# Optimization experiments

Hardware: AMD Instinct MI355X
Metric: run time of the kernel (lower is better)

The kernel has to match this reference:

```python
import jax, jax.numpy as jnp
import numpy as np

NUM_HEADS = 32
NUM_KV_HEADS = 8
HEAD_DIM = 128
ROPE_THETA = 10000.0
MAX_SEQ_LEN = 2048


def build_rope_cache(seq_len, head_dim, theta=10000.0):
    freq_indices = jnp.arange(0, head_dim, 2, dtype=jnp.float32)
    inv_freq = 1.0 / theta ** (freq_indices / head_dim)
    positions = jnp.arange(seq_len, dtype=jnp.float32)
    angles = jnp.outer(positions, inv_freq)  # (S, D/2)
    cos = jnp.cos(angles)
    sin = jnp.sin(angles)
    return jnp.concatenate([cos, cos], axis=-1), jnp.concatenate([sin, sin], axis=-1)


def apply_rotary_embedding(x, cos, sin):
    # x: (B, S, H, D); cos/sin: (S, D)
    d = x.shape[-1]
    x1, x2 = x[..., : d // 2], x[..., d // 2 :]
    x_rot = jnp.concatenate([-x2, x1], axis=-1)
    return x * cos[None, :, None, :] + x_rot * sin[None, :, None, :]


def setup_inputs() -> dict:
    key = jax.random.key(0)
    k_x, k_q, k_k, k_v, k_o = jax.random.split(key, 5)
    B, S, HID = 2, 2048, NUM_HEADS * HEAD_DIM
    KV = NUM_KV_HEADS * HEAD_DIM
    x = jax.random.normal(k_x, (B, S, HID), dtype=jnp.float32)
    # causal mask, shape (B, 1, S, S)
    causal = jnp.tril(jnp.ones((S, S), dtype=bool))
    mask = jnp.broadcast_to(causal[None, None], (B, 1, S, S))
    sc_in = 1.0 / np.sqrt(HID)
    Wq = jax.random.normal(k_q, (HID, HID), dtype=jnp.float32) * sc_in
    Wk = jax.random.normal(k_k, (HID, KV), dtype=jnp.float32) * sc_in
    Wv = jax.random.normal(k_v, (HID, KV), dtype=jnp.float32) * sc_in
    Wo = jax.random.normal(k_o, (HID, HID), dtype=jnp.float32) * sc_in
    return {"x": x, "mask": mask, "Wq": Wq, "Wk": Wk, "Wv": Wv, "Wo": Wo}


def reference(x, mask, Wq, Wk, Wv, Wo):
    B, S, _ = x.shape
    q = (x @ Wq).reshape(B, S, NUM_HEADS, HEAD_DIM)
    k = (x @ Wk).reshape(B, S, NUM_KV_HEADS, HEAD_DIM)
    v = (x @ Wv).reshape(B, S, NUM_KV_HEADS, HEAD_DIM)
    cos, sin = build_rope_cache(MAX_SEQ_LEN, HEAD_DIM, ROPE_THETA)
    cos, sin = cos[:S], sin[:S]
    q = apply_rotary_embedding(q, cos, sin)
    k = apply_rotary_embedding(k, cos, sin)
    group = NUM_HEADS // NUM_KV_HEADS
    if group > 1:
        k = jnp.repeat(k, group, axis=2)
        v = jnp.repeat(v, group, axis=2)
    scale = HEAD_DIM ** -0.5
    # (B, H, S, S)
    scores = jnp.einsum("bqhd,bkhd->bhqk", q, k) * scale
    scores = jnp.where(mask, scores, jnp.finfo(jnp.float32).min)
    attn = jax.nn.softmax(scores, axis=-1)
    out = jnp.einsum("bhqk,bkhd->bqhd", attn, v).reshape(B, S, NUM_HEADS * HEAD_DIM)
    return out @ Wo
```

## Files before the change

### kernel.cpp

```cpp
#include <hip/hip_runtime.h>

#define S_LEN   2048
#define HID_DIM 4096
#define NHEADS  32
#define NKVH    8
#define HD      128
#define KV_DIM  1024
#define KV2     2048
#define BS_ROWS 4096

typedef __attribute__((ext_vector_type(4))) float f32x4;
typedef __attribute__((ext_vector_type(8))) short bf16x8;

__device__ __forceinline__ unsigned short f2b(float f) {
  union { float f; unsigned int u; } cv; cv.f = f;
  unsigned int r = (cv.u + 0x7FFFu + ((cv.u >> 16) & 1u)) >> 16;
  return (unsigned short)r;
}
__device__ __forceinline__ float b2f(unsigned short u) {
  union { unsigned int u; float f; } cv; cv.u = ((unsigned int)u) << 16; return cv.f;
}
__device__ __forceinline__ void gload_lds16(const void* g, void* l) {
  __builtin_amdgcn_global_load_lds(
      (const __attribute__((address_space(1))) unsigned int*)g,
      (__attribute__((address_space(3))) unsigned int*)l, 16, 0, 0);
}
__device__ __forceinline__ float exp2fast(float x) {
#if __has_builtin(__builtin_amdgcn_exp2f)
  return __builtin_amdgcn_exp2f(x);
#else
  return exp2f(x);
#endif
}
__device__ __forceinline__ unsigned cvtpk(float a, float b) {
  unsigned r;
  asm("v_cvt_pk_bf16_f32 %0, %1, %2" : "=v"(r) : "v"(a), "v"(b));
  return r;
}
__device__ __forceinline__ void store_out(float* p, float v) { *p = v; }
__device__ __forceinline__ void store_out(unsigned short* p, float v) { *p = f2b(v); }

__global__ __launch_bounds__(256) void prep_k(const float* __restrict__ x,
                                              unsigned short* __restrict__ xb,
                                              const float* __restrict__ Wq,
                                              unsigned short* __restrict__ wtb,
                                              const float* __restrict__ Wk,
                                              unsigned short* __restrict__ wkt,
                                              const float* __restrict__ Wv,
                                              unsigned short* __restrict__ wvt,
                                              float* __restrict__ cosT,
                                              float* __restrict__ sinT) {
  __shared__ float t[32][33];
  int bid = blockIdx.x;
  const int tid = threadIdx.x;
  if (bid < 16384) {
    int i = bid * 256 + tid;
    f32x4 v = reinterpret_cast<const f32x4*>(x)[i];
    ushort4 o;
    o.x = f2b(v[0]); o.y = f2b(v[1]); o.z = f2b(v[2]); o.w = f2b(v[3]);
    reinterpret_cast<ushort4*>(xb)[i] = o;
    return;
  }
  bid -= 16384;
  const float* W; unsigned short* Wt; int Kd, Nd, bx, by;
  if (bid < 16384) { W = Wq; Wt = wtb; Kd = HID_DIM; Nd = HID_DIM; bx = bid & 127; by = bid >> 7; }
  else {
    bid -= 16384;
    if (bid < 4096) { W = Wk; Wt = wkt; Kd = HID_DIM; Nd = KV_DIM; bx = bid & 31; by = bid >> 5; }
    else {
      bid -= 4096;
      if (bid < 4096) { W = Wv; Wt = wvt; Kd = HID_DIM; Nd = KV_DIM; bx = bid & 31; by = bid >> 5; }
      else {
        bid -= 4096;
        int idx = bid * 256 + tid;
        int s = idx >> 6, i = idx & 63;
        float inv = 1.0f / powf(10000.0f, (float)(2 * i) * (1.0f / 128.0f));
        float ang = (float)s * inv;
        cosT[idx] = cosf(ang);
        sinT[idx] = sinf(ang);
        return;
      }
    }
  }
  const int tx = tid & 31, ty = tid >> 5;
  const int n0 = bx * 32, k0 = by * 32;
#pragma unroll
  for (int i = 0; i < 4; ++i)
    t[ty + 8 * i][tx] = W[(size_t)(k0 + ty + 8 * i) * Nd + n0 + tx];
  __syncthreads();
#pragma unroll
  for (int i = 0; i < 4; ++i)
    Wt[(size_t)(n0 + ty + 8 * i) * Kd + k0 + tx] = f2b(t[tx][ty + 8 * i]);
}

__global__ void transpose_cvt(const float* __restrict__ W, unsigned short* __restrict__ Wt,
                              int K, int N) {
  __shared__ float t[32][33];
  int n0 = blockIdx.x * 32, k0 = blockIdx.y * 32;
  int tx = threadIdx.x, ty = threadIdx.y;
#pragma unroll
  for (int i = 0; i < 4; ++i)
    t[ty + 8 * i][tx] = W[(size_t)(k0 + ty + 8 * i) * N + n0 + tx];
  __syncthreads();
#pragma unroll
  for (int i = 0; i < 4; ++i)
    Wt[(size_t)(n0 + ty + 8 * i) * K + k0 + tx] = f2b(t[tx][ty + 8 * i]);
}

__global__ __launch_bounds__(256) void postkv_k(unsigned short* __restrict__ KVb,
                                                unsigned short* __restrict__ Vt,
                                                const float* __restrict__ cosT,
                                                const float* __restrict__ sinT) {
  __shared__ unsigned short tsh[32][33];
  int bid = blockIdx.x;
  const int tid = threadIdx.x;
  if (bid < 2048) {
    int idx = bid * 256 + tid;
    int i4 = idx & 15;
    int t = idx >> 4;
    int h = t & (NKVH - 1);
    int row = t >> 3;
    int s = row & (S_LEN - 1);
    f32x4 c4 = *reinterpret_cast<const f32x4*>(&cosT[(s << 6) + i4 * 4]);
    f32x4 s4 = *reinterpret_cast<const f32x4*>(&sinT[(s << 6) + i4 * 4]);
    size_t base = (size_t)row * KV2 + (size_t)h * HD + i4 * 4;
    ushort4 xa = *reinterpret_cast<const ushort4*>(&KVb[base]);
    ushort4 xb2 = *reinterpret_cast<const ushort4*>(&KVb[base + 64]);
    unsigned short* pa = (unsigned short*)&xa;
    unsigned short* pb = (unsigned short*)&xb2;
    ushort4 oa, ob;
    unsigned short* qa = (unsigned short*)&oa;
    unsigned short* qb = (unsigned short*)&ob;
#pragma unroll
    for (int j = 0; j < 4; ++j) {
      float x1 = b2f(pa[j]), x2 = b2f(pb[j]);
      qa[j] = f2b(x1 * c4[j] - x2 * s4[j]);
      qb[j] = f2b(x2 * c4[j] + x1 * s4[j]);
    }
    *reinterpret_cast<ushort4*>(&KVb[base])      = oa;
    *reinterpret_cast<ushort4*>(&KVb[base + 64]) = ob;
    return;
  }
  bid -= 2048;
  const int tx = tid & 31, ty = tid >> 5;
  int c0 = (bid & 31) * 32;
  int r0 = (bid >> 5) * 32;
#pragma unroll
  for (int i = 0; i < 4; ++i)
    tsh[ty + 8 * i][tx] = KVb[(size_t)(r0 + ty + 8 * i) * KV2 + KV_DIM + c0 + tx];
  __syncthreads();
  int ob2 = (r0 >> 11) * 1024;
  int oc = r0 & 2047;
#pragma unroll
  for (int i = 0; i < 4; ++i)
    Vt[(size_t)(ob2 + c0 + ty + 8 * i) * S_LEN + oc + tx] = tsh[tx][ty + 8 * i];
}

template <typename OutT>
__global__ __launch_bounds__(256) void gemm_bt(const unsigned short* __restrict__ A,
                                               const unsigned short* __restrict__ Bt,
                                               OutT* __restrict__ C, int M, int N, int K) {
  __shared__ unsigned short As[128 * 32];
  __shared__ unsigned short Bs[128 * 32];
  const int tid = threadIdx.x;
  const int lane = tid & 63;
  const int wave = tid >> 6;
  int nwg = gridDim.x, wg = blockIdx.x;
  int swz = (nwg % 8 == 0) ? ((wg & 7) * (nwg >> 3) + (wg >> 3)) : wg;
  const int nbn = N >> 7;
  const int bm = swz / nbn, bn = swz % nbn;
  const int m0 = bm << 7, n0 = bn << 7;
  const int wr = wave >> 1, wc = wave & 1;
  const int lr = lane & 15, kb = lane >> 4;

  f32x4 acc[4][4];
#pragma unroll
  for (int i = 0; i < 4; ++i)
#pragma unroll
    for (int j = 0; j < 4; ++j) acc[i][j] = (f32x4){0.f, 0.f, 0.f, 0.f};

  const unsigned short* Ab = A + (size_t)m0 * K;
  const unsigned short* Bb = Bt + (size_t)n0 * K;

  for (int k0 = 0; k0 < K; k0 += 32) {
    __syncthreads();
#pragma unroll
    for (int i = 0; i < 2; ++i) {
      int idx = i * 256 + tid;
      int row = idx >> 2;
      int off = (idx & 3) << 3;
      gload_lds16(Ab + (size_t)row * K + k0 + off, As + row * 32 + off);
      gload_lds16(Bb + (size_t)row * K + k0 + off, Bs + row * 32 + off);
    }
    __syncthreads();

    bf16x8 af[4], bfr[4];
#pragma unroll
    for (int mi = 0; mi < 4; ++mi)
      af[mi] = *reinterpret_cast<const bf16x8*>(As + (wr * 64 + mi * 16 + lr) * 32 + kb * 8);
#pragma unroll
    for (int ni = 0; ni < 4; ++ni)
      bfr[ni] = *reinterpret_cast<const bf16x8*>(Bs + (wc * 64 + ni * 16 + lr) * 32 + kb * 8);
#pragma unroll
    for (int mi = 0; mi < 4; ++mi)
#pragma unroll
      for (int ni = 0; ni < 4; ++ni)
        acc[mi][ni] = __builtin_amdgcn_mfma_f32_16x16x32_bf16(af[mi], bfr[ni], acc[mi][ni], 0, 0, 0);
  }

#pragma unroll
  for (int mi = 0; mi < 4; ++mi)
#pragma unroll
    for (int ni = 0; ni < 4; ++ni)
#pragma unroll
      for (int r = 0; r < 4; ++r) {
        int row = m0 + wr * 64 + mi * 16 + kb * 4 + r;
        int col = n0 + wc * 64 + ni * 16 + lr;
        store_out(&C[(size_t)row * N + col], acc[mi][ni][r]);
      }
}

#define STAGE_HALF(dstBase, Sp, k0, h)                                           \
  {                                                                              \
    _Pragma("unroll")                                                            \
    for (int i_ = 0; i_ < 2; ++i_) {                                             \
      int c_ = i_ * 512 + tid;                                                   \
      int rl_ = c_ >> 3, ch_ = c_ & 7;                                           \
      int row_ = (h) * 128 + rl_;                                                \
      gload_lds16((Sp) + (size_t)row_ * K + (k0) + ((ch_ ^ (row_ & 7)) << 3),    \
                  (char*)(dstBase) + row_ * 128 + ch_ * 16);                     \
    }                                                                            \
  }
#define LDF(buf, R, sw) \
  (*reinterpret_cast<const bf16x8*>((const char*)(buf) + (R) * 128 + (sw)))
#define PHASE_SYNC()                                        \
  __builtin_amdgcn_s_barrier();                             \
  asm volatile("s_waitcnt lgkmcnt(0)" ::: "memory");        \
  __builtin_amdgcn_sched_barrier(0);

template <typename OutT>
__global__ __launch_bounds__(512, 1) void gemm256(const unsigned short* __restrict__ A,
                                                  const unsigned short* __restrict__ Bt,
                                                  OutT* __restrict__ C, int M, int N, int K) {
  __shared__ unsigned short Asl[2][256 * 64];
  __shared__ unsigned short Bsl[2][256 * 64];
  const int tid = threadIdx.x;
  const int lane = tid & 63;
  const int wave = tid >> 6;
  const int wr = wave >> 2;
  const int wc = wave & 3;
  const int lr = lane & 15, kb = lane >> 4;

  int nwg = gridDim.x, wg = blockIdx.x;
  int swz = (nwg % 8 == 0) ? ((wg & 7) * (nwg >> 3) + (wg >> 3)) : wg;
  const int nbn = N >> 8;
  const int bm = swz / nbn, bn = swz % nbn;
  const int m0 = bm << 8, n0 = bn << 8;

  const unsigned short* Ab = A + (size_t)m0 * K;
  const unsigned short* Bb = Bt + (size_t)n0 * K;

  f32x4 acc[8][4];
#pragma unroll
  for (int i = 0; i < 8; ++i)
#pragma unroll
    for (int j = 0; j < 4; ++j) acc[i][j] = (f32x4){0.f, 0.f, 0.f, 0.f};

  const int sw0 = ((kb) ^ (lr & 7)) << 4;
  const int sw1 = ((4 + kb) ^ (lr & 7)) << 4;

  STAGE_HALF(Asl[0], Ab, 0, 0); STAGE_HALF(Asl[0], Ab, 0, 1);
  STAGE_HALF(Bsl[0], Bb, 0, 0); STAGE_HALF(Bsl[0], Bb, 0, 1);
  __syncthreads();

  const int nt = K >> 6;
  bf16x8 af[4], bfr[4];

#pragma unroll 1
  for (int t = 0; t < nt; ++t) {
    const unsigned short* Acur = Asl[t & 1];
    const unsigned short* Bcur = Bsl[t & 1];
    unsigned short* Anxt = Asl[(t + 1) & 1];
    unsigned short* Bnxt = Bsl[(t + 1) & 1];
    const int k0n = (t + 1) << 6;
    const bool pf = (t + 1 < nt);

#pragma unroll
    for (int ni = 0; ni < 4; ++ni) bfr[ni] = LDF(Bcur, wc * 64 + ni * 16 + lr, sw0);
#pragma unroll
    for (int mi = 0; mi < 4; ++mi) af[mi] = LDF(Acur, wr * 128 + mi * 16 + lr, sw0);
    if (pf) { STAGE_HALF(Anxt, Ab, k0n, 0); STAGE_HALF(Anxt, Ab, k0n, 1); }
    PHASE_SYNC();
    __builtin_amdgcn_s_setprio(1);
#pragma unroll
    for (int mi = 0; mi < 4; ++mi)
#pragma unroll
      for (int ni = 0; ni < 4; ++ni)
        acc[mi][ni] = __builtin_amdgcn_mfma_f32_16x16x32_bf16(af[mi], bfr[ni], acc[mi][ni], 0, 0, 0);
    __builtin_amdgcn_s_setprio(0);
    __builtin_amdgcn_s_barrier();

#pragma unroll
    for (int mi = 0; mi < 4; ++mi) af[mi] = LDF(Acur, wr * 128 + (mi + 4) * 16 + lr, sw0);
    if (pf) { STAGE_HALF(Bnxt, Bb, k0n, 0); STAGE_HALF(Bnxt, Bb, k0n, 1); }
    PHASE_SYNC();
    __builtin_amdgcn_s_setprio(1);
#pragma unroll
    for (int mi = 0; mi < 4; ++mi)
#pragma unroll
      for (int ni = 0; ni < 4; ++ni)
        acc[mi + 4][ni] = __builtin_amdgcn_mfma_f32_16x16x32_bf16(af[mi], bfr[ni], acc[mi + 4][ni], 0, 0, 0);
    __builtin_amdgcn_s_setprio(0);
    __builtin_amdgcn_s_barrier();

#pragma unroll
    for (int ni = 0; ni < 4; ++ni) bfr[ni] = LDF(Bcur, wc * 64 + ni * 16 + lr, sw1);
#pragma unroll
    for (int mi = 0; mi < 4; ++mi) af[mi] = LDF(Acur, wr * 128 + mi * 16 + lr, sw1);
    PHASE_SYNC();
    __builtin_amdgcn_s_setprio(1);
#pragma unroll
    for (int mi = 0; mi < 4; ++mi)
#pragma unroll
      for (int ni = 0; ni < 4; ++ni)
        acc[mi][ni] = __builtin_amdgcn_mfma_f32_16x16x32_bf16(af[mi], bfr[ni], acc[mi][ni], 0, 0, 0);
    __builtin_amdgcn_s_setprio(0);
    __builtin_amdgcn_s_barrier();

#pragma unroll
    for (int mi = 0; mi < 4; ++mi) af[mi] = LDF(Acur, wr * 128 + (mi + 4) * 16 + lr, sw1);
    PHASE_SYNC();
    __builtin_amdgcn_s_setprio(1);
#pragma unroll
    for (int mi = 0; mi < 4; ++mi)
#pragma unroll
      for (int ni = 0; ni < 4; ++ni)
        acc[mi + 4][ni] = __builtin_amdgcn_mfma_f32_16x16x32_bf16(af[mi], bfr[ni], acc[mi + 4][ni], 0, 0, 0);
    __builtin_amdgcn_s_setprio(0);
    __builtin_amdgcn_s_barrier();

    if (pf) asm volatile("s_waitcnt vmcnt(0)" ::: "memory");
    __builtin_amdgcn_s_barrier();
  }

#pragma unroll
  for (int mi = 0; mi < 8; ++mi)
#pragma unroll
    for (int ni = 0; ni < 4; ++ni)
#pragma unroll
      for (int r = 0; r < 4; ++r) {
        int row = m0 + wr * 128 + mi * 16 + kb * 4 + r;
        int col = n0 + wc * 64 + ni * 16 + lr;
        store_out(&C[(size_t)row * N + col], acc[mi][ni][r]);
      }
}

__global__ __launch_bounds__(256, 2) void attn_fwd(const unsigned short* __restrict__ Q,
                                                   const unsigned short* __restrict__ KV,
                                                   const unsigned short* __restrict__ Vt,
                                                   const float* __restrict__ cosT,
                                                   const float* __restrict__ sinT,
                                                   unsigned short* __restrict__ O) {
  __shared__ unsigned short Ks[2][64 * 128];
  __shared__ unsigned short Ps[4][2][16 * 72];
  const int tid = threadIdx.x, lane = tid & 63, wave = tid >> 6;
  const int lr = lane & 15, kb = lane >> 4;
  const int pr = blockIdx.x;
  const int bh = blockIdx.y;
  const int b = bh >> 5, h = bh & 31, kvh = h >> 2;
  const unsigned short* Qp = Q + (size_t)b * S_LEN * HID_DIM + (size_t)h * HD;
  const unsigned short* Kp = KV + (size_t)b * S_LEN * KV2 + (size_t)kvh * HD;
  const unsigned short* Vtp = Vt + (size_t)(b * 8 + kvh) * HD * S_LEN;
  unsigned short* Op = O + (size_t)b * S_LEN * HID_DIM + (size_t)h * HD;

#pragma unroll 1
  for (int pass = 0; pass < 2; ++pass) {
    const int qt = pass ? pr : 15 - pr;
    const int q0 = qt * 128;
    int qrowQ[2];
    qrowQ[0] = q0 + wave * 32 + lr;
    qrowQ[1] = q0 + wave * 32 + 16 + lr;

    bf16x8 qf[2][4];
#pragma unroll
    for (int qs = 0; qs < 2; ++qs) {
      const int qrow = qrowQ[qs];
      bf16x8 raw[4];
#pragma unroll
      for (int dc = 0; dc < 4; ++dc)
        raw[dc] = *reinterpret_cast<const bf16x8*>(Qp + (size_t)qrow * HID_DIM + dc * 32 + kb * 8);
      const float* ct = cosT + (qrow << 6) + kb * 8;
      const float* st = sinT + (qrow << 6) + kb * 8;
      f32x4 cv0 = *(const f32x4*)(ct),      cv1 = *(const f32x4*)(ct + 4);
      f32x4 cv2 = *(const f32x4*)(ct + 32), cv3 = *(const f32x4*)(ct + 36);
      f32x4 sv0 = *(const f32x4*)(st),      sv1 = *(const f32x4*)(st + 4);
      f32x4 sv2 = *(const f32x4*)(st + 32), sv3 = *(const f32x4*)(st + 36);
      const float sc = 0.08838834764831843f * 1.4426950408889634f;
#pragma unroll
      for (int j = 0; j < 8; ++j) {
        const int jj = j & 3;
        float c0 = (j < 4) ? cv0[jj] : cv1[jj];
        float s0 = (j < 4) ? sv0[jj] : sv1[jj];
        float c1 = (j < 4) ? cv2[jj] : cv3[jj];
        float s1 = (j < 4) ? sv2[jj] : sv3[jj];
        float a1 = b2f((unsigned short)raw[0][j]), a2 = b2f((unsigned short)raw[2][j]);
        qf[qs][0][j] = (short)f2b((a1 * c0 - a2 * s0) * sc);
        qf[qs][2][j] = (short)f2b((a2 * c0 + a1 * s0) * sc);
        float b1 = b2f((unsigned short)raw[1][j]), b2x = b2f((unsigned short)raw[3][j]);
        qf[qs][1][j] = (short)f2b((b1 * c1 - b2x * s1) * sc);
        qf[qs][3][j] = (short)f2b((b2x * c1 + b1 * s1) * sc);
      }
    }

    f32x4 of[2][8];
#pragma unroll
    for (int qs = 0; qs < 2; ++qs)
#pragma unroll
      for (int i = 0; i < 8; ++i) of[qs][i] = (f32x4){0.f, 0.f, 0.f, 0.f};
    float mrow[2] = {-3.0e38f, -3.0e38f};
    float lrow[2] = {0.f, 0.f};

    const int nsteps = 2 * qt + 2;

#pragma unroll
    for (int i = 0; i < 4; ++i) {
      int c = i * 256 + tid;
      int key = c >> 4;
      int ch = (c & 15) ^ (key & 7);
      gload_lds16(Kp + (size_t)key * KV2 + ch * 8, &Ks[0][0] + c * 8);
    }
    __syncthreads();

#pragma unroll 1
    for (int t = 0; t < nsteps; ++t) {
      const int kv0 = t << 6;
      const unsigned short* Kcur = &Ks[t & 1][0];
      const bool active = (kv0 <= q0 + wave * 32 + 31);

      bf16x8 vf0[8], vf1[8];
      if (active) {
#pragma unroll
        for (int dc2 = 0; dc2 < 8; ++dc2) {
          const unsigned short* vr = Vtp + (size_t)(dc2 * 16 + lr) * S_LEN + kv0 + kb * 8;
          vf0[dc2] = *reinterpret_cast<const bf16x8*>(vr);
          vf1[dc2] = *reinterpret_cast<const bf16x8*>(vr + 32);
        }
      }

      if (t + 1 < nsteps) {
        unsigned short* Knxt = &Ks[(t + 1) & 1][0];
#pragma unroll
        for (int i = 0; i < 4; ++i) {
          int c = i * 256 + tid;
          int key = c >> 4;
          int ch = (c & 15) ^ (key & 7);
          gload_lds16(Kp + (size_t)(kv0 + 64 + key) * KV2 + ch * 8, Knxt + c * 8);
        }
      }

      if (active) {
        f32x4 sf[2][4];
#pragma unroll
        for (int qs = 0; qs < 2; ++qs)
#pragma unroll
          for (int ki = 0; ki < 4; ++ki) sf[qs][ki] = (f32x4){0.f, 0.f, 0.f, 0.f};
#pragma unroll
        for (int ki = 0; ki < 4; ++ki)
#pragma unroll
          for (int dc = 0; dc < 4; ++dc) {
            bf16x8 kf = *reinterpret_cast<const bf16x8*>(
                Kcur + (ki * 16 + lr) * 128 + (((dc * 4 + kb) ^ (lr & 7)) << 3));
            sf[0][ki] = __builtin_amdgcn_mfma_f32_16x16x32_bf16(kf, qf[0][dc], sf[0][ki], 0, 0, 0);
            sf[1][ki] = __builtin_amdgcn_mfma_f32_16x16x32_bf16(kf, qf[1][dc], sf[1][ki], 0, 0, 0);
          }

#pragma unroll
        for (int qs = 0; qs < 2; ++qs) {
          if (kv0 + 63 > q0 + wave * 32 + qs * 16) {
            const int thr = qrowQ[qs] - kv0;
#pragma unroll
            for (int ki = 0; ki < 4; ++ki)
#pragma unroll
              for (int r = 0; r < 4; ++r)
                if (ki * 16 + kb * 4 + r > thr) sf[qs][ki][r] = -3.0e38f;
          }
        }

        {
          const int qs = 0;
          float m8 = -3.0e38f;
#pragma unroll
          for (int ki = 0; ki < 4; ++ki)
#pragma unroll
            for (int r = 0; r < 4; ++r) m8 = fmaxf(m8, sf[qs][ki][r]);
          m8 = fmaxf(m8, __shfl_xor(m8, 16));
          m8 = fmaxf(m8, __shfl_xor(m8, 32));
          if (__any(m8 > mrow[qs] + 11.5f)) {
            float mn = fmaxf(mrow[qs], m8);
            float corr = exp2fast(mrow[qs] - mn);
            lrow[qs] *= corr;
#pragma unroll
            for (int r = 0; r < 4; ++r) {
              float cr = __shfl(corr, kb * 4 + r);
#pragma unroll
              for (int dc2 = 0; dc2 < 8; ++dc2) of[qs][dc2][r] *= cr;
            }
            mrow[qs] = mn;
          }
          float rs = 0.f;
#pragma unroll
          for (int ki = 0; ki < 4; ++ki) {
            float p0 = exp2fast(sf[qs][ki][0] - mrow[qs]);
            float p1 = exp2fast(sf[qs][ki][1] - mrow[qs]);
            float p2 = exp2fast(sf[qs][ki][2] - mrow[qs]);
            float p3 = exp2fast(sf[qs][ki][3] - mrow[qs]);
            rs += (p0 + p1) + (p2 + p3);
            uint2 w;
            w.x = cvtpk(p0, p1);
            w.y = cvtpk(p2, p3);
            *reinterpret_cast<uint2*>(&Ps[wave][qs][lr * 72 + ki * 16 + kb * 4]) = w;
          }
          rs += __shfl_xor(rs, 16);
          rs += __shfl_xor(rs, 32);
          lrow[qs] += rs;
        }
        asm volatile("s_waitcnt lgkmcnt(0)" ::: "memory");
        __builtin_amdgcn_sched_barrier(0);

        {
          bf16x8 pfA = *reinterpret_cast<const bf16x8*>(&Ps[wave][0][lr * 72 + kb * 8]);
          bf16x8 pfB = *reinterpret_cast<const bf16x8*>(&Ps[wave][0][lr * 72 + 32 + kb * 8]);
#pragma unroll
          for (int dc2 = 0; dc2 < 8; ++dc2) {
            of[0][dc2] = __builtin_amdgcn_mfma_f32_16x16x32_bf16(pfA, vf0[dc2], of[0][dc2], 0, 0, 0);
            of[0][dc2] = __builtin_amdgcn_mfma_f32_16x16x32_bf16(pfB, vf1[dc2], of[0][dc2], 0, 0, 0);
          }
        }

        {
          const int qs = 1;
          float m8 = -3.0e38f;
#pragma unroll
          for (int ki = 0; ki < 4; ++ki)
#pragma unroll
            for (int r = 0; r < 4; ++r) m8 = fmaxf(m8, sf[qs][ki][r]);
          m8 = fmaxf(m8, __shfl_xor(m8, 16));
          m8 = fmaxf(m8, __shfl_xor(m8, 32));
          if (__any(m8 > mrow[qs] + 11.5f)) {
            float mn = fmaxf(mrow[qs], m8);
            float corr = exp2fast(mrow[qs] - mn);
            lrow[qs] *= corr;
#pragma unroll
            for (int r = 0; r < 4; ++r) {
              float cr = __shfl(corr, kb * 4 + r);
#pragma unroll
              for (int dc2 = 0; dc2 < 8; ++dc2) of[qs][dc2][r] *= cr;
            }
            mrow[qs] = mn;
          }
          float rs = 0.f;
#pragma unroll
          for (int ki = 0; ki < 4; ++ki) {
            float p0 = exp2fast(sf[qs][ki][0] - mrow[qs]);
            float p1 = exp2fast(sf[qs][ki][1] - mrow[qs]);
            float p2 = exp2fast(sf[qs][ki][2] - mrow[qs]);
            float p3 = exp2fast(sf[qs][ki][3] - mrow[qs]);
            rs += (p0 + p1) + (p2 + p3);
            uint2 w;
            w.x = cvtpk(p0, p1);
            w.y = cvtpk(p2, p3);
            *reinterpret_cast<uint2*>(&Ps[wave][qs][lr * 72 + ki * 16 + kb * 4]) = w;
          }
          rs += __shfl_xor(rs, 16);
          rs += __shfl_xor(rs, 32);
          lrow[qs] += rs;
        }
        asm volatile("s_waitcnt lgkmcnt(0)" ::: "memory");
        __builtin_amdgcn_sched_barrier(0);

        {
          bf16x8 pfC = *reinterpret_cast<const bf16x8*>(&Ps[wave][1][lr * 72 + kb * 8]);
          bf16x8 pfD = *reinterpret_cast<const bf16x8*>(&Ps[wave][1][lr * 72 + 32 + kb * 8]);
#pragma unroll
          for (int dc2 = 0; dc2 < 8; ++dc2) {
            of[1][dc2] = __builtin_amdgcn_mfma_f32_16x16x32_bf16(pfC, vf0[dc2], of[1][dc2], 0, 0, 0);
            of[1][dc2] = __builtin_amdgcn_mfma_f32_16x16x32_bf16(pfD, vf1[dc2], of[1][dc2], 0, 0, 0);
          }
        }
      }

      __syncthreads();
    }

#pragma unroll
    for (int qs = 0; qs < 2; ++qs) {
      float linv[4];
#pragma unroll
      for (int r = 0; r < 4; ++r) linv[r] = 1.0f / __shfl(lrow[qs], kb * 4 + r);
#pragma unroll
      for (int dc2 = 0; dc2 < 8; ++dc2)
#pragma unroll
        for (int r = 0; r < 4; ++r) {
          int qg = q0 + wave * 32 + qs * 16 + kb * 4 + r;
          Op[(size_t)qg * HID_DIM + dc2 * 16 + lr] = f2b(of[qs][dc2][r] * linv[r]);
        }
    }
  }
}

extern "C" void kernel_launch(void* const* d_in, const int* in_sizes, int n_in,
                              void* d_out, int out_size, void* d_ws, size_t ws_size,
                              hipStream_t stream) {
  const float* x  = (const float*)d_in[0];
  const float* Wq = (const float*)d_in[2];
  const float* Wk = (const float*)d_in[3];
  const float* Wv = (const float*)d_in[4];
  const float* Wo = (const float*)d_in[5];
  float* out = (float*)d_out;

  char* ws = (char*)d_ws;
  unsigned short* xb  = (unsigned short*)(ws + 0);
  unsigned short* wtb = (unsigned short*)(ws + 33554432);
  unsigned short* wkt = (unsigned short*)(ws + 67108864);
  unsigned short* wvt = (unsigned short*)(ws + 75497472);
  unsigned short* Qb  = (unsigned short*)(ws + 83886080);
  unsigned short* KVb = (unsigned short*)(ws + 117440512);
  float* cosT = (float*)(ws + 134217728);
  float* sinT = (float*)(ws + 134742016);
  unsigned short* AO  = xb;
  unsigned short* Vtb = wkt;

  prep_k<<<41472, 256, 0, stream>>>(x, xb, Wq, wtb, Wk, wkt, Wv, wvt, cosT, sinT);

  gemm256<unsigned short><<<256, 512, 0, stream>>>(xb, wtb, Qb, BS_ROWS, HID_DIM, HID_DIM);
  gemm_bt<unsigned short><<<512, 256, 0, stream>>>(xb, wkt, KVb, BS_ROWS, KV2, HID_DIM);

  transpose_cvt<<<dim3(128, 128), dim3(32, 8), 0, stream>>>(Wo, wtb, HID_DIM, HID_DIM);
  postkv_k<<<6144, 256, 0, stream>>>(KVb, Vtb, cosT, sinT);

  attn_fwd<<<dim3(8, 64), 256, 0, stream>>>(Qb, KVb, Vtb, cosT, sinT, AO);

  gemm256<float><<<256, 512, 0, stream>>>(AO, wtb, out, BS_ROWS, HID_DIM, HID_DIM);
}
```

Baseline: 554.6 us.

## Fold Wo transpose into postkv kernel and restructure attention PV loop

Merges the standalone Wo transpose/convert launch into the postkv kernel as extra blocks, removing one kernel launch. In attention, the per-wave causal 'active' guard is removed, softmax for both query sub-tiles is computed before the PV matmul, and V fragments are loaded in two halves of 32 keys so only eight V registers are live at a time. The PV MFMAs for both sub-tiles are interleaved on shared V fragments. This aims to lower register pressure and launch overhead, at the cost of doing masked work for waves that are fully above the diagonal.

```diff
diff --git a/kernel.cpp b/kernel.cpp
--- a/kernel.cpp
+++ b/kernel.cpp
@@ -43,11 +43,11 @@
 __global__ __launch_bounds__(256) void prep_k(const float* __restrict__ x,
                                               unsigned short* __restrict__ xb,
                                               const float* __restrict__ Wq,
-                                              unsigned short* __restrict__ wtb,
+                                              unsigned short* __restrict__ wtq,
                                               const float* __restrict__ Wk,
-                                              unsigned short* __restrict__ wkt,
+                                              unsigned short* __restrict__ wtk,
                                               const float* __restrict__ Wv,
-                                              unsigned short* __restrict__ wvt,
+                                              unsigned short* __restrict__ wtv,
                                               float* __restrict__ cosT,
                                               float* __restrict__ sinT) {
   __shared__ float t[32][33];
@@ -62,14 +62,14 @@
     return;
   }
   bid -= 16384;
-  const float* W; unsigned short* Wt; int Kd, Nd, bx, by;
-  if (bid < 16384) { W = Wq; Wt = wtb; Kd = HID_DIM; Nd = HID_DIM; bx = bid & 127; by = bid >> 7; }
+  const float* W; unsigned short* Wt; int Nd, bx, by;
+  if (bid < 16384) { W = Wq; Wt = wtq; Nd = HID_DIM; bx = bid & 127; by = bid >> 7; }
   else {
     bid -= 16384;
-    if (bid < 4096) { W = Wk; Wt = wkt; Kd = HID_DIM; Nd = KV_DIM; bx = bid & 31; by = bid >> 5; }
+    if (bid < 4096) { W = Wk; Wt = wtk; Nd = KV_DIM; bx = bid & 31; by = bid >> 5; }
     else {
       bid -= 4096;
-      if (bid < 4096) { W = Wv; Wt = wvt; Kd = HID_DIM; Nd = KV_DIM; bx = bid & 31; by = bid >> 5; }
+      if (bid < 4096) { W = Wv; Wt = wtv; Nd = KV_DIM; bx = bid & 31; by = bid >> 5; }
       else {
         bid -= 4096;
         int idx = bid * 256 + tid;
@@ -90,27 +90,16 @@
   __syncthreads();
 #pragma unroll
   for (int i = 0; i < 4; ++i)
-    Wt[(size_t)(n0 + ty + 8 * i) * Kd + k0 + tx] = f2b(t[tx][ty + 8 * i]);
-}
-
-__global__ void transpose_cvt(const float* __restrict__ W, unsigned short* __restrict__ Wt,
-                              int K, int N) {
-  __shared__ float t[32][33];
-  int n0 = blockIdx.x * 32, k0 = blockIdx.y * 32;
-  int tx = threadIdx.x, ty = threadIdx.y;
-#pragma unroll
-  for (int i = 0; i < 4; ++i)
-    t[ty + 8 * i][tx] = W[(size_t)(k0 + ty + 8 * i) * N + n0 + tx];
-  __syncthreads();
-#pragma unroll
-  for (int i = 0; i < 4; ++i)
-    Wt[(size_t)(n0 + ty + 8 * i) * K + k0 + tx] = f2b(t[tx][ty + 8 * i]);
+    Wt[(size_t)(n0 + ty + 8 * i) * HID_DIM + k0 + tx] = f2b(t[tx][ty + 8 * i]);
 }
 
 __global__ __launch_bounds__(256) void postkv_k(unsigned short* __restrict__ KVb,
                                                 unsigned short* __restrict__ Vt,
+                                                const float* __restrict__ Wo,
+                                                unsigned short* __restrict__ woT,
                                                 const float* __restrict__ cosT,
                                                 const float* __restrict__ sinT) {
+  __shared__ float tf[32][33];
   __shared__ unsigned short tsh[32][33];
   int bid = blockIdx.x;
   const int tid = threadIdx.x;
@@ -143,17 +132,31 @@
   }
   bid -= 2048;
   const int tx = tid & 31, ty = tid >> 5;
-  int c0 = (bid & 31) * 32;
-  int r0 = (bid >> 5) * 32;
-#pragma unroll
-  for (int i = 0; i < 4; ++i)
-    tsh[ty + 8 * i][tx] = KVb[(size_t)(r0 + ty + 8 * i) * KV2 + KV_DIM + c0 + tx];
-  __syncthreads();
-  int ob2 = (r0 >> 11) * 1024;
-  int oc = r0 & 2047;
-#pragma unroll
-  for (int i = 0; i < 4; ++i)
-    Vt[(size_t)(ob2 + c0 + ty + 8 * i) * S_LEN + oc + tx] = tsh[tx][ty + 8 * i];
+  if (bid < 4096) {
+    int c0 = (bid & 31) * 32;
+    int r0 = (bid >> 5) * 32;
+#pragma unroll
+    for (int i = 0; i < 4; ++i)
+      tsh[ty + 8 * i][tx] = KVb[(size_t)(r0 + ty + 8 * i) * KV2 + KV_DIM + c0 + tx];
+    __syncthreads();
+    int ob2 = (r0 >> 11) * 1024;
+    int oc = r0 & 2047;
+#pragma unroll
+    for (int i = 0; i < 4; ++i)
+      Vt[(size_t)(ob2 + c0 + ty + 8 * i) * S_LEN + oc + tx] = tsh[tx][ty + 8 * i];
+    return;
+  }
+  bid -= 4096;
+  {
+    int n0 = (bid & 127) * 32, k0 = (bid >> 7) * 32;
+#pragma unroll
+    for (int i = 0; i < 4; ++i)
+      tf[ty + 8 * i][tx] = Wo[(size_t)(k0 + ty + 8 * i) * HID_DIM + n0 + tx];
+    __syncthreads();
+#pragma unroll
+    for (int i = 0; i < 4; ++i)
+      woT[(size_t)(n0 + ty + 8 * i) * HID_DIM + k0 + tx] = f2b(tf[tx][ty + 8 * i]);
+  }
 }
 
 template <typename OutT>
@@ -435,17 +438,12 @@
     for (int t = 0; t < nsteps; ++t) {
       const int kv0 = t << 6;
       const unsigned short* Kcur = &Ks[t & 1][0];
-      const bool active = (kv0 <= q0 + wave * 32 + 31);
-
-      bf16x8 vf0[8], vf1[8];
-      if (active) {
-#pragma unroll
-        for (int dc2 = 0; dc2 < 8; ++dc2) {
-          const unsigned short* vr = Vtp + (size_t)(dc2 * 16 + lr) * S_LEN + kv0 + kb * 8;
-          vf0[dc2] = *reinterpret_cast<const bf16x8*>(vr);
-          vf1[dc2] = *reinterpret_cast<const bf16x8*>(vr + 32);
-        }
-      }
+
+      bf16x8 vf[8];
+#pragma unroll
+      for (int dc2 = 0; dc2 < 8; ++dc2)
+        vf[dc2] = *reinterpret_cast<const bf16x8*>(
+            Vtp + (size_t)(dc2 * 16 + lr) * S_LEN + kv0 + kb * 8);
 
       if (t + 1 < nsteps) {
         unsigned short* Knxt = &Ks[(t + 1) & 1][0];
@@ -458,134 +456,94 @@
         }
       }
 
-      if (active) {
-        f32x4 sf[2][4];
-#pragma unroll
-        for (int qs = 0; qs < 2; ++qs)
-#pragma unroll
-          for (int ki = 0; ki < 4; ++ki) sf[qs][ki] = (f32x4){0.f, 0.f, 0.f, 0.f};
+      f32x4 sf[2][4];
+#pragma unroll
+      for (int qs = 0; qs < 2; ++qs)
+#pragma unroll
+        for (int ki = 0; ki < 4; ++ki) sf[qs][ki] = (f32x4){0.f, 0.f, 0.f, 0.f};
+#pragma unroll
+      for (int ki = 0; ki < 4; ++ki)
+#pragma unroll
+        for (int dc = 0; dc < 4; ++dc) {
+          bf16x8 kf = *reinterpret_cast<const bf16x8*>(
+              Kcur + (ki * 16 + lr) * 128 + (((dc * 4 + kb) ^ (lr & 7)) << 3));
+          sf[0][ki] = __builtin_amdgcn_mfma_f32_16x16x32_bf16(kf, qf[0][dc], sf[0][ki], 0, 0, 0);
+          sf[1][ki] = __builtin_amdgcn_mfma_f32_16x16x32_bf16(kf, qf[1][dc], sf[1][ki], 0, 0, 0);
+        }
+
+#pragma unroll
+      for (int qs = 0; qs < 2; ++qs) {
+        if (kv0 + 63 > q0 + wave * 32 + qs * 16) {
+          const int thr = qrowQ[qs] - kv0;
+#pragma unroll
+          for (int ki = 0; ki < 4; ++ki)
+#pragma unroll
+            for (int r = 0; r < 4; ++r)
+              if (ki * 16 + kb * 4 + r > thr) sf[qs][ki][r] = -3.0e38f;
+        }
+      }
+
+#pragma unroll
+      for (int qs = 0; qs < 2; ++qs) {
+        float m8 = -3.0e38f;
 #pragma unroll
         for (int ki = 0; ki < 4; ++ki)
 #pragma unroll
-          for (int dc = 0; dc < 4; ++dc) {
-            bf16x8 kf = *reinterpret_cast<const bf16x8*>(
-                Kcur + (ki * 16 + lr) * 128 + (((dc * 4 + kb) ^ (lr & 7)) << 3));
-            sf[0][ki] = __builtin_amdgcn_mfma_f32_16x16x32_bf16(kf, qf[0][dc], sf[0][ki], 0, 0, 0);
-            sf[1][ki] = __builtin_amdgcn_mfma_f32_16x16x32_bf16(kf, qf[1][dc], sf[1][ki], 0, 0, 0);
+          for (int r = 0; r < 4; ++r) m8 = fmaxf(m8, sf[qs][ki][r]);
+        m8 = fmaxf(m8, __shfl_xor(m8, 16));
+        m8 = fmaxf(m8, __shfl_xor(m8, 32));
+        if (__any(m8 > mrow[qs] + 11.5f)) {
+          float mn = fmaxf(mrow[qs], m8);
+          float corr = exp2fast(mrow[qs] - mn);
+          lrow[qs] *= corr;
+#pragma unroll
+          for (int r = 0; r < 4; ++r) {
+            float cr = __shfl(corr, kb * 4 + r);
+#pragma unroll
+            for (int dc2 = 0; dc2 < 8; ++dc2) of[qs][dc2][r] *= cr;
           }
-
-#pragma unroll
-        for (int qs = 0; qs < 2; ++qs) {
-          if (kv0 + 63 > q0 + wave * 32 + qs * 16) {
-            const int thr = qrowQ[qs] - kv0;
-#pragma unroll
-            for (int ki = 0; ki < 4; ++ki)
-#pragma unroll
-              for (int r = 0; r < 4; ++r)
-                if (ki * 16 + kb * 4 + r > thr) sf[qs][ki][r] = -3.0e38f;
-          }
-        }
-
-        {
-          const int qs = 0;
-          float m8 = -3.0e38f;
-#pragma unroll
-          for (int ki = 0; ki < 4; ++ki)
-#pragma unroll
-            for (int r = 0; r < 4; ++r) m8 = fmaxf(m8, sf[qs][ki][r]);
-          m8 = fmaxf(m8, __shfl_xor(m8, 16));
-          m8 = fmaxf(m8, __shfl_xor(m8, 32));
-          if (__any(m8 > mrow[qs] + 11.5f)) {
-            float mn = fmaxf(mrow[qs], m8);
-            float corr = exp2fast(mrow[qs] - mn);
-            lrow[qs] *= corr;
-#pragma unroll
-            for (int r = 0; r < 4; ++r) {
-              float cr = __shfl(corr, kb * 4 + r);
-#pragma unroll
-              for (int dc2 = 0; dc2 < 8; ++dc2) of[qs][dc2][r] *= cr;
-            }
-            mrow[qs] = mn;
-          }
-          float rs = 0.f;
-#pragma unroll
-          for (int ki = 0; ki < 4; ++ki) {
-            float p0 = exp2fast(sf[qs][ki][0] - mrow[qs]);
-            float p1 = exp2fast(sf[qs][ki][1] - mrow[qs]);
-            float p2 = exp2fast(sf[qs][ki][2] - mrow[qs]);
-            float p3 = exp2fast(sf[qs][ki][3] - mrow[qs]);
-            rs += (p0 + p1) + (p2 + p3);
-            uint2 w;
-            w.x = cvtpk(p0, p1);
-            w.y = cvtpk(p2, p3);
-            *reinterpret_cast<uint2*>(&Ps[wave][qs][lr * 72 + ki * 16 + kb * 4]) = w;
-          }
-          rs += __shfl_xor(rs, 16);
-          rs += __shfl_xor(rs, 32);
-          lrow[qs] += rs;
-        }
-        asm volatile("s_waitcnt lgkmcnt(0)" ::: "memory");
-        __builtin_amdgcn_sched_barrier(0);
-
-        {
-          bf16x8 pfA = *reinterpret_cast<const bf16x8*>(&Ps[wave][0][lr * 72 + kb * 8]);
-          bf16x8 pfB = *reinterpret_cast<const bf16x8*>(&Ps[wave][0][lr * 72 + 32 + kb * 8]);
-#pragma unroll
-          for (int dc2 = 0; dc2 < 8; ++dc2) {
-            of[0][dc2] = __builtin_amdgcn_mfma_f32_16x16x32_bf16(pfA, vf0[dc2], of[0][dc2], 0, 0, 0);
-            of[0][dc2] = __builtin_amdgcn_mfma_f32_16x16x32_bf16(pfB, vf1[dc2], of[0][dc2], 0, 0, 0);
-          }
-        }
-
-        {
-          const int qs = 1;
-          float m8 = -3.0e38f;
-#pragma unroll
-          for (int ki = 0; ki < 4; ++ki)
-#pragma unroll
-            for (int r = 0; r < 4; ++r) m8 = fmaxf(m8, sf[qs][ki][r]);
-          m8 = fmaxf(m8, __shfl_xor(m8, 16));
-          m8 = fmaxf(m8, __shfl_xor(m8, 32));
-          if (__any(m8 > mrow[qs] + 11.5f)) {
-            float mn = fmaxf(mrow[qs], m8);
-            float corr = exp2fast(mrow[qs] - mn);
-            lrow[qs] *= corr;
-#pragma unroll
-            for (int r = 0; r < 4; ++r) {
-              float cr = __shfl(corr, kb * 4 + r);
-#pragma unroll
-              for (int dc2 = 0; dc2 < 8; ++dc2) of[qs][dc2][r] *= cr;
-            }
-            mrow[qs] = mn;
-          }
-          float rs = 0.f;
-#pragma unroll
-          for (int ki = 0; ki < 4; ++ki) {
-            float p0 = exp2fast(sf[qs][ki][0] - mrow[qs]);
-            float p1 = exp2fast(sf[qs][ki][1] - mrow[qs]);
-            float p2 = exp2fast(sf[qs][ki][2] - mrow[qs]);
-            float p3 = exp2fast(sf[qs][ki][3] - mrow[qs]);
-            rs += (p0 + p1) + (p2 + p3);
-            uint2 w;
-            w.x = cvtpk(p0, p1);
-            w.y = cvtpk(p2, p3);
-            *reinterpret_cast<uint2*>(&Ps[wave][qs][lr * 72 + ki * 16 + kb * 4]) = w;
-          }
-          rs += __shfl_xor(rs, 16);
-          rs += __shfl_xor(rs, 32);
-          lrow[qs] += rs;
-        }
-        asm volatile("s_waitcnt lgkmcnt(0)" ::: "memory");
-        __builtin_amdgcn_sched_barrier(0);
-
-        {
-          bf16x8 pfC = *reinterpret_cast<const bf16x8*>(&Ps[wave][1][lr * 72 + kb * 8]);
-          bf16x8 pfD = *reinterpret_cast<const bf16x8*>(&Ps[wave][1][lr * 72 + 32 + kb * 8]);
-#pragma unroll
-          for (int dc2 = 0; dc2 < 8; ++dc2) {
-            of[1][dc2] = __builtin_amdgcn_mfma_f32_16x16x32_bf16(pfC, vf0[dc2], of[1][dc2], 0, 0, 0);
-            of[1][dc2] = __builtin_amdgcn_mfma_f32_16x16x32_bf16(pfD, vf1[dc2], of[1][dc2], 0, 0, 0);
-          }
+          mrow[qs] = mn;
+        }
+        float rs = 0.f;
+#pragma unroll
+        for (int ki = 0; ki < 4; ++ki) {
+          float p0 = exp2fast(sf[qs][ki][0] - mrow[qs]);
+          float p1 = exp2fast(sf[qs][ki][1] - mrow[qs]);
+          float p2 = exp2fast(sf[qs][ki][2] - mrow[qs]);
+          float p3 = exp2fast(sf[qs][ki][3] - mrow[qs]);
+          rs += (p0 + p1) + (p2 + p3);
+          uint2 w;
+          w.x = cvtpk(p0, p1);
+          w.y = cvtpk(p2, p3);
+          *reinterpret_cast<uint2*>(&Ps[wave][qs][lr * 72 + ki * 16 + kb * 4]) = w;
+        }
+        rs += __shfl_xor(rs, 16);
+        rs += __shfl_xor(rs, 32);
+        lrow[qs] += rs;
+      }
+      asm volatile("s_waitcnt lgkmcnt(0)" ::: "memory");
+      __builtin_amdgcn_sched_barrier(0);
+
+      {
+        bf16x8 pf0 = *reinterpret_cast<const bf16x8*>(&Ps[wave][0][lr * 72 + kb * 8]);
+        bf16x8 pf1 = *reinterpret_cast<const bf16x8*>(&Ps[wave][1][lr * 72 + kb * 8]);
+#pragma unroll
+        for (int dc2 = 0; dc2 < 8; ++dc2) {
+          of[0][dc2] = __builtin_amdgcn_mfma_f32_16x16x32_bf16(pf0, vf[dc2], of[0][dc2], 0, 0, 0);
+          of[1][dc2] = __builtin_amdgcn_mfma_f32_16x16x32_bf16(pf1, vf[dc2], of[1][dc2], 0, 0, 0);
+        }
+      }
+#pragma unroll
+      for (int dc2 = 0; dc2 < 8; ++dc2)
+        vf[dc2] = *reinterpret_cast<const bf16x8*>(
+            Vtp + (size_t)(dc2 * 16 + lr) * S_LEN + kv0 + 32 + kb * 8);
+      {
+        bf16x8 pf0 = *reinterpret_cast<const bf16x8*>(&Ps[wave][0][lr * 72 + 32 + kb * 8]);
+        bf16x8 pf1 = *reinterpret_cast<const bf16x8*>(&Ps[wave][1][lr * 72 + 32 + kb * 8]);
+#pragma unroll
+        for (int dc2 = 0; dc2 < 8; ++dc2) {
+          of[0][dc2] = __builtin_amdgcn_mfma_f32_16x16x32_bf16(pf0, vf[dc2], of[0][dc2], 0, 0, 0);
+          of[1][dc2] = __builtin_amdgcn_mfma_f32_16x16x32_bf16(pf1, vf[dc2], of[1][dc2], 0, 0, 0);
         }
       }
 
@@ -629,16 +587,16 @@
   float* sinT = (float*)(ws + 134742016);
   unsigned short* AO  = xb;
   unsigned short* Vtb = wkt;
+  unsigned short* woT = wtb;
 
   prep_k<<<41472, 256, 0, stream>>>(x, xb, Wq, wtb, Wk, wkt, Wv, wvt, cosT, sinT);
 
   gemm256<unsigned short><<<256, 512, 0, stream>>>(xb, wtb, Qb, BS_ROWS, HID_DIM, HID_DIM);
   gemm_bt<unsigned short><<<512, 256, 0, stream>>>(xb, wkt, KVb, BS_ROWS, KV2, HID_DIM);
 
-  transpose_cvt<<<dim3(128, 128), dim3(32, 8), 0, stream>>>(Wo, wtb, HID_DIM, HID_DIM);
-  postkv_k<<<6144, 256, 0, stream>>>(KVb, Vtb, cosT, sinT);
+  postkv_k<<<22528, 256, 0, stream>>>(KVb, Vtb, Wo, woT, cosT, sinT);
 
   attn_fwd<<<dim3(8, 64), 256, 0, stream>>>(Qb, KVb, Vtb, cosT, sinT, AO);
 
-  gemm256<float><<<256, 512, 0, stream>>>(AO, wtb, out, BS_ROWS, HID_DIM, HID_DIM);
-}
+  gemm256<float><<<256, 512, 0, stream>>>(AO, woT, out, BS_ROWS, HID_DIM, HID_DIM);
+}
```

Result: faster. 543.5 us (median of 2 runs) (-2.0%).
